# Kernel optimization log

Hardware: AMD Instinct MI355X
Metric: run time of the kernel (lower is better)

Reference implementation:

```python
import jax, jax.numpy as jnp
import numpy as np

D = 128           # volume / particle box size (pixels)
B = 8             # particles per batch
K = 125           # SO(3) grid poses (5x5x5 around each center Euler)
TOPK = 2          # keep_top_k_values
MAX_SHIFT_FRAC = 0.25  # main_config.projmatching.max_shift_fraction


def setup_inputs() -> dict:
    key = jax.random.key(0)
    k1, k2, k3, k4 = jax.random.split(key, 4)
    vol = jax.random.normal(k1, (D, D, D), dtype=jnp.float32)
    parts = jax.random.normal(k2, (B, D, D), dtype=jnp.float32)
    ctf = jax.random.uniform(k3, (B, D, D // 2 + 1), dtype=jnp.float32)
    euler_degs = jax.random.normal(k4, (K, 3), dtype=jnp.float32) * 8.0
    return {"vol": vol, "parts": parts, "ctf": ctf, "euler_degs": euler_degs}


def _rot_z(t):
    c, s = jnp.cos(t), jnp.sin(t)
    z, o = jnp.zeros_like(t), jnp.ones_like(t)
    return jnp.stack([jnp.stack([c, -s, z], -1),
                      jnp.stack([s, c, z], -1),
                      jnp.stack([z, z, o], -1)], -2)


def _rot_y(t):
    c, s = jnp.cos(t), jnp.sin(t)
    z, o = jnp.zeros_like(t), jnp.ones_like(t)
    return jnp.stack([jnp.stack([c, z, s], -1),
                      jnp.stack([z, o, z], -1),
                      jnp.stack([-s, z, c], -1)], -2)


def euler_zyz_to_matrix(degs):
    # RELION Euler convention ZYZ: R = Rz(a) @ Ry(b) @ Rz(c)
    rad = jnp.deg2rad(degs)
    return _rot_z(rad[..., 0]) @ _rot_y(rad[..., 1]) @ _rot_z(rad[..., 2])


def trilinear_sample(vol, zi, yi, xi):
    # vol: (Dz, Dy, W) complex64; coords: (K, h, w) float32 array indices
    Dz, Dy, W = vol.shape
    z0, y0, x0 = jnp.floor(zi), jnp.floor(yi), jnp.floor(xi)
    tz, ty, tx = zi - z0, yi - y0, xi - x0
    out = jnp.zeros(zi.shape, dtype=vol.dtype)
    for dz in (0, 1):
        wz = tz if dz else 1.0 - tz
        zc = z0 + dz
        vz = (zc >= 0) & (zc < Dz)
        zdx = jnp.clip(zc, 0, Dz - 1).astype(jnp.int32)
        for dy in (0, 1):
            wy = ty if dy else 1.0 - ty
            yc = y0 + dy
            vy = (yc >= 0) & (yc < Dy)
            ydx = jnp.clip(yc, 0, Dy - 1).astype(jnp.int32)
            for dx in (0, 1):
                wx = tx if dx else 1.0 - tx
                xc = x0 + dx
                vx = (xc >= 0) & (xc < W)
                xdx = jnp.clip(xc, 0, W - 1).astype(jnp.int32)
                w = jnp.where(vz & vy & vx, wz * wy * wx, 0.0)
                out = out + w * vol[zdx, ydx, xdx]
    return out


def project_fourier(vol_rfft, rotmats):
    # extract_central_slices_rfft: pose-dependent gather+trilinear interp of a
    # central slice from the fftshifted 3D rfft volume. Output: (K, D, D//2+1).
    d = D
    w = d // 2 + 1
    y = jnp.arange(d, dtype=jnp.float32) - d // 2   # fftshifted full-dim freqs (pixel units)
    x = jnp.arange(w, dtype=jnp.float32)            # rfft (non-negative) freqs
    yy, xx = jnp.meshgrid(y, x, indexing='ij')      # (d, w)
    coords = jnp.stack([xx, yy, jnp.zeros_like(yy)], -1)       # xyz, (d, w, 3), z = 0 plane
    rot = jnp.einsum('kij,hwj->khwi', rotmats, coords)          # (K, d, w, 3) rotated xyz
    conj_mask = rot[..., 0] < 0                                  # Hermitian symmetry: flip to x>=0 half
    rot = jnp.where(conj_mask[..., None], -rot, rot)
    xi = rot[..., 0]
    yi = rot[..., 1] + d // 2
    zi = rot[..., 2] + d // 2
    samples = trilinear_sample(vol_rfft, zi, yi, xi)
    samples = jnp.where(conj_mask, jnp.conj(samples), samples)
    r2 = xx ** 2 + yy ** 2                                       # zero beyond Nyquist radius
    samples = jnp.where(r2[None] > (d // 2) ** 2, 0.0, samples)
    return samples


def reference(vol, parts, ctf, euler_degs):
    # compute_dft: rfft volume, fftshift non-rfft dims
    vol_rfft = jnp.fft.fftshift(jnp.fft.rfftn(vol), axes=(0, 1))
    parts_rfft = jnp.fft.fftshift(jnp.fft.rfft2(parts), axes=(-2,))  # (B, D, W)
    rotmats = euler_zyz_to_matrix(euler_degs)                        # (K, 3, 3)
    projs = project_fourier(vol_rfft, rotmats)                       # (K, D, W)
    projs = ctf[:, None] * projs[None]                               # _apply_ctfF: (B, K, D, W)
    # correlate_dft_2d: cross-correlation via iFFT of parts * conj(projs)
    prod = parts_rfft[:, None] * jnp.conj(projs)
    prod = jnp.fft.ifftshift(prod, axes=(-2,))
    corr = jnp.fft.irfft2(prod, s=(D, D))                            # (B, K, D, D)
    corr = jnp.fft.fftshift(corr, axes=(-2, -1))                     # zero shift at center
    # _extract_ccor_max: restrict to |shift| <= max_shift_fraction*D, take top-k peaks
    center = D // 2
    max_shift = int(MAX_SHIFT_FRAC * D)
    idx = jnp.arange(D) - center
    win = (jnp.abs(idx)[:, None] <= max_shift) & (jnp.abs(idx)[None, :] <= max_shift)
    masked = jnp.where(win, corr, -jnp.inf)
    flat = masked.reshape(B, K, D * D)
    vals, top_idx = jax.lax.top_k(flat, TOPK)                        # (B, K, TOPK)
    shifts = jnp.stack([top_idx // D - center, top_idx % D - center], -1)  # (B, K, TOPK, 2) yx
    return vals, shifts
```

## Files before the change

### kernel.cpp

```cpp
#include <hip/hip_runtime.h>
#include <math.h>

#define D 128
#define W 65
#define NK 125
#define NB 8
#define SLAB (D*W)
#define TWO_PI 6.28318530717958647692f
#define R2C 0.70710678118654752440f
#define C8C 0.92387953251128675613f
#define S8C 0.38268343236508977173f


__device__ __forceinline__ bool better(float va, int ia, float vb, int ib) {
    return (va > vb) || (va == vb && ia < ib);
}
__device__ __forceinline__ float2 cmul(float2 a, float2 b) {
    return make_float2(a.x*b.x - a.y*b.y, a.x*b.y + a.y*b.x);
}
__device__ __forceinline__ void cmac(float2& acc, float2 a, float2 b) {
    acc.x = fmaf(a.x, b.x, fmaf(-a.y, b.y, acc.x));
    acc.y = fmaf(a.x, b.y, fmaf( a.y, b.x, acc.y));
}
__device__ __forceinline__ float2 cadd(float2 a, float2 b){ return make_float2(a.x+b.x, a.y+b.y); }
__device__ __forceinline__ float2 csub(float2 a, float2 b){ return make_float2(a.x-b.x, a.y-b.y); }

__device__ __forceinline__ void fft8_fwd(const float2* x, float2* a) {
    float2 e0 = x[0], o0 = x[1], e1 = x[2], o1 = x[3];
    float2 e2 = x[4], o2 = x[5], e3 = x[6], o3 = x[7];
    float2 t0 = cadd(e0, e2), t1 = csub(e0, e2);
    float2 t2 = cadd(e1, e3), t3 = csub(e1, e3);
    float2 E0 = cadd(t0, t2), E2 = csub(t0, t2);
    float2 E1 = make_float2(t1.x + t3.y, t1.y - t3.x);
    float2 E3 = make_float2(t1.x - t3.y, t1.y + t3.x);
    float2 u0 = cadd(o0, o2), u1 = csub(o0, o2);
    float2 u2 = cadd(o1, o3), u3 = csub(o1, o3);
    float2 O0 = cadd(u0, u2), O2 = csub(u0, u2);
    float2 O1 = make_float2(u1.x + u3.y, u1.y - u3.x);
    float2 O3 = make_float2(u1.x - u3.y, u1.y + u3.x);
    float2 w1 = make_float2(R2C*(O1.x + O1.y), R2C*(O1.y - O1.x));
    float2 w2 = make_float2(O2.y, -O2.x);
    float2 w3 = make_float2(R2C*(O3.y - O3.x), -R2C*(O3.x + O3.y));
    a[0] = cadd(E0, O0); a[4] = csub(E0, O0);
    a[1] = cadd(E1, w1); a[5] = csub(E1, w1);
    a[2] = cadd(E2, w2); a[6] = csub(E2, w2);
    a[3] = cadd(E3, w3); a[7] = csub(E3, w3);
}


template<int MODE>
__device__ __forceinline__ void fft128v2(const float* __restrict__ inf,
                                         const float2* __restrict__ inc,
                                         float2* __restrict__ out,
                                         int l0, int nlines,
                                         float2* __restrict__ Fl,
                                         float2* __restrict__ twf) {
    int tid = threadIdx.x;
    int line, t;
    if (MODE == 0) { t = tid & 7; line = tid >> 3; }
    else           { line = tid & 31; t = tid >> 5; }
    int l = l0 + line;
    bool live = (l < nlines);

    if (tid < 128) {
        float s, c;
        sincosf(-TWO_PI * (float)tid / 128.0f, &s, &c);
        twf[tid] = make_float2(c, s);
    }

    int base = 0, stride = 1;
    if (MODE == 1 || MODE == 3) { base = (l / W) * SLAB + (l % W); stride = W; }
    else if (MODE == 2) { base = l; stride = SLAB; }

    float2 xe[8], xo[8];
    if (live) {
        if (MODE == 0) {
            const float* r = inf + (size_t)l * D;
            #pragma unroll
            for (int j = 0; j < 8; ++j) {
                xe[j] = make_float2(r[t + 16*j], 0.f);
                xo[j] = make_float2(r[t + 8 + 16*j], 0.f);
            }
        } else {
            #pragma unroll
            for (int j = 0; j < 8; ++j) {
                xe[j] = inc[base + (t + 16*j) * stride];
                xo[j] = inc[base + (t + 8 + 16*j) * stride];
            }
        }
    } else {
        #pragma unroll
        for (int j = 0; j < 8; ++j) { xe[j] = make_float2(0,0); xo[j] = make_float2(0,0); }
    }
    float2 E[8], O[8];
    fft8_fwd(xe, E);
    fft8_fwd(xo, O);
    {
        const float2 w16[8] = {
            { 1.f, 0.f }, { C8C, -S8C }, { R2C, -R2C }, { S8C, -C8C },
            { 0.f, -1.f }, { -S8C, -C8C }, { -R2C, -R2C }, { -C8C, -S8C }
        };
        float2* Fp = Fl + line * 137 + t * 17;
        #pragma unroll
        for (int kk = 0; kk < 8; ++kk) {
            float2 wo = cmul(w16[kk], O[kk]);
            Fp[kk]     = cadd(E[kk], wo);
            Fp[kk + 8] = csub(E[kk], wo);
        }
    }
    __syncthreads();
    if (live) {
        const float2* Fr = Fl + line * 137;
        #pragma unroll
        for (int s = 0; s < 16; ++s) {
            int slot = t + 8 * s;
            if (MODE == 0 && slot > 64) break;
            int k = (MODE == 0) ? slot : (slot ^ 64);
            int kk = k & 15;
            float2 acc = make_float2(0.f, 0.f);
            #pragma unroll
            for (int tt = 0; tt < 8; ++tt) {
                cmac(acc, Fr[tt * 17 + kk], twf[(tt * k) & 127]);
            }
            if (MODE == 0)      out[(size_t)l * W + slot] = acc;
            else if (MODE == 3) out[(size_t)l * D + slot] = acc;
            else                out[base + slot * stride] = acc;
        }
    }
}


__global__ __launch_bounds__(256) void k1_kernel(const float* __restrict__ vol,
                                                 const float* __restrict__ parts,
                                                 const float* __restrict__ ctf,
                                                 const float* __restrict__ euler,
                                                 float2* __restrict__ bufA,
                                                 float2* __restrict__ pT1,
                                                 float* __restrict__ CT,
                                                 float* __restrict__ rot) {
    __shared__ float2 Fl[32 * 137];
    __shared__ float2 twf[128];
    int bid = blockIdx.x;
    int tid = threadIdx.x;
    if (bid < 512) {
        fft128v2<0>(vol, nullptr, bufA, bid * 32, D*D, Fl, twf);
    } else if (bid < 544) {
        fft128v2<0>(parts, nullptr, pT1, (bid - 512) * 32, NB*D, Fl, twf);
    } else if (bid == 544) {
        int k = tid;
        if (k < NK) {
            const float d2r = 0.017453292519943295f;
            float a = euler[k*3+0]*d2r, b = euler[k*3+1]*d2r, c = euler[k*3+2]*d2r;
            float sa, ca, sb, cb, sc, cc;
            sincosf(a, &sa, &ca); sincosf(b, &sb, &cb); sincosf(c, &sc, &cc);
            rot[k*9+0] =  ca*cb*cc - sa*sc;
            rot[k*9+1] = -ca*cb*sc - sa*cc;
            rot[k*9+2] =  ca*sb;
            rot[k*9+3] =  sa*cb*cc + ca*sc;
            rot[k*9+4] = -sa*cb*sc + ca*cc;
            rot[k*9+5] =  sa*sb;
            rot[k*9+6] = -sb*cc;
            rot[k*9+7] =  sb*sc;
            rot[k*9+8] =  cb;
        }
    } else {
        int i = (bid - 545) * 256 + tid;
        if (i < NB * W * D) {
            int m = i & (D-1);
            int t2 = i >> 7;
            int x = t2 % W;
            int b = t2 / W;
            CT[i] = ctf[b * SLAB + m * W + x];
        }
    }
}

__global__ __launch_bounds__(256) void k2_kernel(const float2* __restrict__ bufA,
                                                 float2* __restrict__ bufB,
                                                 const float2* __restrict__ pT1,
                                                 float2* __restrict__ QT) {
    __shared__ float2 Fl[32 * 137];
    __shared__ float2 twf[128];
    int bid = blockIdx.x;
    if (bid < 260) fft128v2<1>(nullptr, bufA, bufB, bid * 32, D*W, Fl, twf);
    else           fft128v2<3>(nullptr, pT1, QT, (bid - 260) * 32, NB*W, Fl, twf);
}

__global__ __launch_bounds__(256) void k3_kernel(const float2* __restrict__ bufB,
                                                 float2* __restrict__ bufA) {
    __shared__ float2 Fl[32 * 137];
    __shared__ float2 twf[128];
    fft128v2<2>(nullptr, bufB, bufA, blockIdx.x * 32, SLAB, Fl, twf);
}


__global__ void proj_kernel(const float2* __restrict__ vol, const float* __restrict__ rot,
                            float2* __restrict__ projT) {
    int idx = blockIdx.x * blockDim.x + threadIdx.x;
    if (idx >= NK * D * W) return;
    int h = idx & (D-1);
    int t2 = idx >> 7;
    int w = t2 % W;
    int k = t2 / W;
    float x = (float)w;
    float y = (float)(h - 64);
    const float* R = rot + k*9;
    float rx = R[0]*x + R[1]*y;
    float ry = R[3]*x + R[4]*y;
    float rz = R[6]*x + R[7]*y;
    bool neg = rx < 0.0f;
    if (neg) { rx = -rx; ry = -ry; rz = -rz; }
    float xi = rx;
    float yi = ry + 64.0f;
    float zi = rz + 64.0f;
    float z0 = floorf(zi), y0 = floorf(yi), x0 = floorf(xi);
    float tz = zi - z0, ty = yi - y0, tx = xi - x0;
    int z0i = (int)z0, y0i = (int)y0, x0i = (int)x0;
    float ar = 0.f, ai = 0.f;
    for (int dz = 0; dz < 2; ++dz) {
        float wz = dz ? tz : 1.0f - tz;
        int zc = z0i + dz;
        bool vz = (zc >= 0) && (zc < D);
        int zx = min(max(zc, 0), D-1);
        for (int dy = 0; dy < 2; ++dy) {
            float wy = dy ? ty : 1.0f - ty;
            int yc = y0i + dy;
            bool vy = (yc >= 0) && (yc < D);
            int yx = min(max(yc, 0), D-1);
            for (int dx = 0; dx < 2; ++dx) {
                float wx = dx ? tx : 1.0f - tx;
                int xc = x0i + dx;
                bool vx = (xc >= 0) && (xc < W);
                int xx = min(max(xc, 0), W-1);
                float wt = (vz && vy && vx) ? wz*wy*wx : 0.0f;
                float2 v = vol[zx * SLAB + yx * W + xx];
                ar = fmaf(wt, v.x, ar);
                ai = fmaf(wt, v.y, ai);
            }
        }
    }
    if (neg) ai = -ai;
    int yy = h - 64;
    if (w*w + yy*yy > 4096) { ar = 0.f; ai = 0.f; }
    projT[idx] = make_float2(ar, ai);
}


__global__ __launch_bounds__(256, 2) void corr_kernel(const float2* __restrict__ QT,
                                                      const float*  __restrict__ CT,
                                                      const float2* __restrict__ PJT,
                                                      float* __restrict__ outv) {
    __shared__ float2 tw[128];
    __shared__ float2 Ab[17*144];
    __shared__ float2 BC[32*67];
    __shared__ float  Ny[65];
    __shared__ float  redv[8];
    __shared__ int    redi[8];

    int bk = blockIdx.x;
    int b = bk / NK;
    int k = bk - b * NK;
    int tid = threadIdx.x;
    const float inv_d = 1.0f / 128.0f;

    if (tid < 128) {
        float s, c;
        sincosf(TWO_PI * (float)tid / 128.0f, &s, &c);
        tw[tid] = make_float2(c, s);
    }

    const float2* Qb = QT + b * (W * D);
    const float*  Cb = CT + b * (W * D);
    const float2* Jk = PJT + k * (W * D);

    int lane = tid & 63;
    int wv = tid >> 6;
    int sv = lane & 7;
    int vp = (96 + lane) & 127;
    float acc[16];
    #pragma unroll
    for (int j = 0; j < 16; ++j) acc[j] = 0.0f;
    float accR = 0.0f;
    int ur = 0, vr = 0;
    if (tid < 129) { if (tid < 65) { ur = 64; vr = tid; } else { ur = tid - 65; vr = 64; } }

    __syncthreads();

    float2 wvp = tw[vp];
    float2 tq = make_float2(1.0f, 0.0f);

    for (int cg = 0; cg < 4; ++cg) {
        int ncol = (cg == 0) ? 17 : 16;
        for (int i = tid; i < ncol * 16; i += 256) {
            int l = i >> 4, m0 = i & 15;
            int x = (l < 16) ? (4*cg + (l >> 2) + 16 * (l & 3)) : 64;
            const float2* Qx = Qb + x * 128 + m0;
            const float*  Cx = Cb + x * 128 + m0;
            const float2* Jx = Jk + x * 128 + m0;
            float2 p[8];
            #pragma unroll
            for (int j = 0; j < 8; ++j) {
                float2 qv = Qx[16*j];
                float  cf = Cx[16*j];
                float2 pj = Jx[16*j];
                float sx = qv.x * cf, sy = qv.y * cf;
                p[j] = make_float2(sx*pj.x + sy*pj.y, sy*pj.x - sx*pj.y);
            }
            float2 e0 = p[0], o0 = p[1], e1 = p[2], o1 = p[3];
            float2 e2 = p[4], o2 = p[5], e3 = p[6], o3 = p[7];
            float2 t0 = cadd(e0, e2), t1 = csub(e0, e2);
            float2 t2 = cadd(e1, e3), t3 = csub(e1, e3);
            float2 E0 = cadd(t0, t2), E2 = csub(t0, t2);
            float2 E1 = make_float2(t1.x - t3.y, t1.y + t3.x);
            float2 E3 = make_float2(t1.x + t3.y, t1.y - t3.x);
            float2 u0 = cadd(o0, o2), u1 = csub(o0, o2);
            float2 u2 = cadd(o1, o3), u3 = csub(o1, o3);
            float2 O0 = cadd(u0, u2), O2 = csub(u0, u2);
            float2 O1 = make_float2(u1.x - u3.y, u1.y + u3.x);
            float2 O3 = make_float2(u1.x + u3.y, u1.y - u3.x);
            float2 w1o = make_float2(R2C*(O1.x - O1.y), R2C*(O1.x + O1.y));
            float2 w2o = make_float2(-O2.y, O2.x);
            float2 w3o = make_float2(R2C*(-O3.x - O3.y), R2C*(O3.x - O3.y));
            float2* A = Ab + l * 144 + m0;
            A[0*18] = cadd(E0, O0);
            A[4*18] = csub(E0, O0);
            A[1*18] = cadd(E1, w1o);
            A[5*18] = csub(E1, w1o);
            A[2*18] = cadd(E2, w2o);
            A[6*18] = csub(E2, w2o);
            A[3*18] = cadd(E3, w3o);
            A[7*18] = csub(E3, w3o);
        }
        __syncthreads();
        {
            int lim = (cg == 0) ? 325 : 260;
            for (int i = tid; i < lim; i += 256) {
                if (i < 260) {
                    int q = i / 65;
                    int u2 = i - q * 65;
                    int r = u2 & 7, up = (96 + u2) & 127;
                    float2 wup = tw[up];
                    const float4* A0 = (const float4*)(Ab + (4*q+0)*144 + r*18);
                    const float4* A1 = (const float4*)(Ab + (4*q+1)*144 + r*18);
                    const float4* A2 = (const float4*)(Ab + (4*q+2)*144 + r*18);
                    const float4* A3 = (const float4*)(Ab + (4*q+3)*144 + r*18);
                    float2 g0{0,0}, g1{0,0}, g2{0,0}, g3{0,0};
                    float2 tc = make_float2(1.0f, 0.0f);
                    #pragma unroll
                    for (int h = 0; h < 8; ++h) {
                        float2 tA = tc;
                        float2 tB = cmul(tA, wup);
                        tc = cmul(tB, wup);
                        float4 a;
                        a = A0[h]; cmac(g0, make_float2(a.x,a.y), tA); cmac(g0, make_float2(a.z,a.w), tB);
                        a = A1[h]; cmac(g1, make_float2(a.x,a.y), tA); cmac(g1, make_float2(a.z,a.w), tB);
                        a = A2[h]; cmac(g2, make_float2(a.x,a.y), tA); cmac(g2, make_float2(a.z,a.w), tB);
                        a = A3[h]; cmac(g3, make_float2(a.x,a.y), tA); cmac(g3, make_float2(a.z,a.w), tB);
                    }
                    float sg = (u2 & 1) ? -inv_d : inv_d;
                    g0.x *= sg; g0.y *= sg; g1.x *= sg; g1.y *= sg;
                    g2.x *= sg; g2.y *= sg; g3.x *= sg; g3.y *= sg;
                    if (cg == 0 && q == 0) { g0.x *= 0.5f; g0.y *= 0.5f; }
                    float2 h0 = g0, h1 = g1, h2 = g2, h3 = g3;
                    const float sc = 2.0f * inv_d;
                    float2 p1 = make_float2(R2C*(h1.x - h1.y), R2C*(h1.x + h1.y));
                    float2 q1 = make_float2(R2C*(-h1.x - h1.y), R2C*(h1.x - h1.y));
                    float2 i1 = make_float2(-h1.y, h1.x);
                    float2 i2 = make_float2(-h2.y, h2.x);
                    float2 n2 = make_float2( h2.y, -h2.x);
                    float2 p3 = make_float2(R2C*(h3.x - h3.y), R2C*(h3.x + h3.y));
                    float2 q3 = make_float2(R2C*(-h3.x - h3.y), R2C*(h3.x - h3.y));
                    float2 i3 = make_float2(-h3.y, h3.x);
                    float2 a02 = cadd(h0, h2), s02 = csub(h0, h2);
                    float2 s0 = cadd(a02, cadd(h1, h3));
                    float2 s4 = csub(a02, cadd(h1, h3));
                    float2 s2 = cadd(s02, csub(i1, i3));
                    float2 s6 = csub(s02, csub(i1, i3));
                    float2 b0i = cadd(h0, i2);
                    float2 b0n = cadd(h0, n2);
                    float2 s1 = cadd(b0i, cadd(p1, q3));
                    float2 s5 = csub(b0i, cadd(p1, q3));
                    float2 s3 = cadd(b0n, cadd(q1, p3));
                    float2 s7 = csub(b0n, cadd(q1, p3));
                    float2* Bp = BC + q * (8*67) + u2;
                    Bp[0*67] = make_float2(s0.x*sc, s0.y*sc);
                    Bp[1*67] = make_float2(s1.x*sc, s1.y*sc);
                    Bp[2*67] = make_float2(s2.x*sc, s2.y*sc);
                    Bp[3*67] = make_float2(s3.x*sc, s3.y*sc);
                    Bp[4*67] = make_float2(s4.x*sc, s4.y*sc);
                    Bp[5*67] = make_float2(s5.x*sc, s5.y*sc);
                    Bp[6*67] = make_float2(s6.x*sc, s6.y*sc);
                    Bp[7*67] = make_float2(s7.x*sc, s7.y*sc);
                } else {
                    int u2 = i - 260;
                    int r = u2 & 7, up = (96 + u2) & 127;
                    float2 wup = tw[up];
                    const float4* A = (const float4*)(Ab + 16*144 + r*18);
                    float re = 0.0f;
                    float2 tc = make_float2(1.0f, 0.0f);
                    #pragma unroll
                    for (int h = 0; h < 8; ++h) {
                        float2 tA = tc;
                        float2 tB = cmul(tA, wup);
                        tc = cmul(tB, wup);
                        float4 a = A[h];
                        re = fmaf(a.x, tA.x, fmaf(-a.y, tA.y, re));
                        re = fmaf(a.z, tB.x, fmaf(-a.w, tB.y, re));
                    }
                    Ny[u2] = ((u2 & 1) ? -inv_d : inv_d) * re;
                }
            }
        }
        __syncthreads();
        {
            #pragma unroll
            for (int q = 0; q < 4; ++q) {
                const float2* Bq = BC + (q * 8 + sv) * 67 + wv * 16;
                float tx = tq.x, ty = tq.y;
                #pragma unroll
                for (int j = 0; j < 16; ++j) {
                    float2 bv = Bq[j];
                    acc[j] = fmaf(bv.x, tx, fmaf(-bv.y, ty, acc[j]));
                }
                tq = cmul(tq, wvp);
            }
            if (cg == 0) {
                float sgn = (lane & 1) ? -inv_d : inv_d;
                #pragma unroll
                for (int j = 0; j < 16; ++j) acc[j] = fmaf(sgn, Ny[wv * 16 + j], acc[j]);
            }
            if (tid < 129) {
                int sr = vr & 7, vpr = (96 + vr) & 127;
                float a = accR;
                #pragma unroll
                for (int q = 0; q < 4; ++q) {
                    float2 t = tw[((4*cg + q) * vpr) & 127];
                    float2 bv = BC[(q * 8 + sr) * 67 + ur];
                    a = fmaf(bv.x, t.x, fmaf(-bv.y, t.y, a));
                }
                if (cg == 0) a += (vr & 1) ? -inv_d * Ny[ur] : inv_d * Ny[ur];
                accR = a;
            }
        }
        __syncthreads();
    }

    float v1 = -INFINITY, v2 = -INFINITY;
    int i1 = 0x7fffffff, i2 = 0x7fffffff;
    #pragma unroll
    for (int j = 0; j < 16; ++j) {
        float val = acc[j];
        int uu = wv * 16 + j;
        int fl = (32 + uu) * D + (32 + lane);
        if (better(val, fl, v1, i1)) { v2 = v1; i2 = i1; v1 = val; i1 = fl; }
        else if (better(val, fl, v2, i2)) { v2 = val; i2 = fl; }
    }
    if (tid < 129) {
        int fl = (32 + ur) * D + (32 + vr);
        if (better(accR, fl, v1, i1)) { v2 = v1; i2 = i1; v1 = accR; i1 = fl; }
        else if (better(accR, fl, v2, i2)) { v2 = accR; i2 = fl; }
    }
    for (int off = 32; off > 0; off >>= 1) {
        float b1 = __shfl_down(v1, off); int j1 = __shfl_down(i1, off);
        float b2 = __shfl_down(v2, off); int j2 = __shfl_down(i2, off);
        if (better(b1, j1, v1, i1)) {
            float nv2; int ni2;
            if (better(v1, i1, b2, j2)) { nv2 = v1; ni2 = i1; } else { nv2 = b2; ni2 = j2; }
            v1 = b1; i1 = j1; v2 = nv2; i2 = ni2;
        } else {
            if (better(b1, j1, v2, i2)) { v2 = b1; i2 = j1; }
        }
    }
    int wave = tid >> 6;
    if ((tid & 63) == 0) {
        redv[wave*2]   = v1; redi[wave*2]   = i1;
        redv[wave*2+1] = v2; redi[wave*2+1] = i2;
    }
    __syncthreads();
    if (tid == 0) {
        float r1 = -INFINITY, r2 = -INFINITY;
        int q1 = 0x7fffffff, q2 = 0x7fffffff;
        for (int i = 0; i < 8; ++i) {
            float val = redv[i]; int fl = redi[i];
            if (better(val, fl, r1, q1)) { r2 = r1; q2 = q1; r1 = val; q1 = fl; }
            else if (better(val, fl, r2, q2)) { r2 = val; q2 = fl; }
        }
        int base = bk * 2;
        outv[base]     = r1;
        outv[base + 1] = r2;
        float* os = outv + NB*NK*2;
        os[(base    )*2 + 0] = (float)(q1 / D - 64);
        os[(base    )*2 + 1] = (float)(q1 % D - 64);
        os[(base + 1)*2 + 0] = (float)(q2 / D - 64);
        os[(base + 1)*2 + 1] = (float)(q2 % D - 64);
    }
}


extern "C" void kernel_launch(void* const* d_in, const int* in_sizes, int n_in,
                              void* d_out, int out_size, void* d_ws, size_t ws_size,
                              hipStream_t stream) {
    const float* vol   = (const float*)d_in[0];
    const float* parts = (const float*)d_in[1];
    const float* ctf   = (const float*)d_in[2];
    const float* euler = (const float*)d_in[3];
    float* out = (float*)d_out;

    const int VOLC = D * SLAB;
    float2* bufA   = (float2*)d_ws;
    float2* bufB   = bufA + VOLC;
    float2* pT1    = bufB + VOLC;
    float2* QT     = pT1 + NB * SLAB;
    float2* PJT    = QT + NB * W * D;
    float*  CT     = (float*)(PJT + NK * W * D);
    float*  rot    = CT + NB * W * D;

    k1_kernel<<<805, 256, 0, stream>>>(vol, parts, ctf, euler, bufA, pT1, CT, rot);
    k2_kernel<<<277, 256, 0, stream>>>(bufA, bufB, pT1, QT);
    k3_kernel<<<260, 256, 0, stream>>>(bufB, bufA);
    proj_kernel<<<(NK*D*W + 255) / 256, 256, 0, stream>>>(bufA, rot, PJT);
    corr_kernel<<<NB * NK, 256, 0, stream>>>(QT, CT, PJT, out);
}
```

Measured before the change: 92.95 us.

## Prefetch next column group into registers and remap blocks for L2 reuse

The corr kernel now loads the Q, CTF and projection values for the next column group into registers right after the barrier, so the global loads overlap the DFT stage that works from shared memory. Block indices are remapped so that consecutive blocks share the same projection k across the batch index, which is meant to improve L2 reuse of the projection data. The twiddle recurrence now steps by the squared twiddle, which shortens the dependency chain. The register prefetch raises register pressure under launch_bounds(256,2) and could cause spills.

```diff
diff --git a/kernel.cpp b/kernel.cpp
--- a/kernel.cpp
+++ b/kernel.cpp
@@ -45,6 +45,34 @@
     a[1] = cadd(E1, w1); a[5] = csub(E1, w1);
     a[2] = cadd(E2, w2); a[6] = csub(E2, w2);
     a[3] = cadd(E3, w3); a[7] = csub(E3, w3);
+}
+
+__device__ __forceinline__ void ifft8_store(float2* __restrict__ Ab, const float2* p,
+                                            int l, int m0) {
+    float2 e0 = p[0], o0 = p[1], e1 = p[2], o1 = p[3];
+    float2 e2 = p[4], o2 = p[5], e3 = p[6], o3 = p[7];
+    float2 t0 = cadd(e0, e2), t1 = csub(e0, e2);
+    float2 t2 = cadd(e1, e3), t3 = csub(e1, e3);
+    float2 E0 = cadd(t0, t2), E2 = csub(t0, t2);
+    float2 E1 = make_float2(t1.x - t3.y, t1.y + t3.x);
+    float2 E3 = make_float2(t1.x + t3.y, t1.y - t3.x);
+    float2 u0 = cadd(o0, o2), u1 = csub(o0, o2);
+    float2 u2 = cadd(o1, o3), u3 = csub(o1, o3);
+    float2 O0 = cadd(u0, u2), O2 = csub(u0, u2);
+    float2 O1 = make_float2(u1.x - u3.y, u1.y + u3.x);
+    float2 O3 = make_float2(u1.x + u3.y, u1.y - u3.x);
+    float2 w1o = make_float2(R2C*(O1.x - O1.y), R2C*(O1.x + O1.y));
+    float2 w2o = make_float2(-O2.y, O2.x);
+    float2 w3o = make_float2(R2C*(-O3.x - O3.y), R2C*(O3.x - O3.y));
+    float2* A = Ab + l * 144 + m0;
+    A[0*18] = cadd(E0, O0);
+    A[4*18] = csub(E0, O0);
+    A[1*18] = cadd(E1, w1o);
+    A[5*18] = csub(E1, w1o);
+    A[2*18] = cadd(E2, w2o);
+    A[6*18] = csub(E2, w2o);
+    A[3*18] = cadd(E3, w3o);
+    A[7*18] = csub(E3, w3o);
 }
 
 
@@ -257,9 +285,10 @@
     __shared__ float  redv[8];
     __shared__ int    redi[8];
 
-    int bk = blockIdx.x;
-    int b = bk / NK;
-    int k = bk - b * NK;
+    int g = blockIdx.x;
+    int logical = (g & 7) * 125 + (g >> 3);
+    int k = logical >> 3;
+    int b = logical & 7;
     int tid = threadIdx.x;
     const float inv_d = 1.0f / 128.0f;
 
@@ -289,49 +318,50 @@
     float2 wvp = tw[vp];
     float2 tq = make_float2(1.0f, 0.0f);
 
+    int l1 = tid >> 4, m01 = tid & 15;
+    float2 Qv[8]; float Cv[8]; float2 Jv[8];
+
     for (int cg = 0; cg < 4; ++cg) {
-        int ncol = (cg == 0) ? 17 : 16;
-        for (int i = tid; i < ncol * 16; i += 256) {
-            int l = i >> 4, m0 = i & 15;
-            int x = (l < 16) ? (4*cg + (l >> 2) + 16 * (l & 3)) : 64;
-            const float2* Qx = Qb + x * 128 + m0;
-            const float*  Cx = Cb + x * 128 + m0;
-            const float2* Jx = Jk + x * 128 + m0;
+        if (cg == 0) {
+            for (int i = tid; i < 17 * 16; i += 256) {
+                int l = i >> 4, m0 = i & 15;
+                int x = (l < 16) ? ((l >> 2) + 16 * (l & 3)) : 64;
+                const float2* Qx = Qb + x * 128 + m0;
+                const float*  Cx = Cb + x * 128 + m0;
+                const float2* Jx = Jk + x * 128 + m0;
+                float2 p[8];
+                #pragma unroll
+                for (int j = 0; j < 8; ++j) {
+                    float2 qv = Qx[16*j];
+                    float  cf = Cx[16*j];
+                    float2 pj = Jx[16*j];
+                    float sx = qv.x * cf, sy = qv.y * cf;
+                    p[j] = make_float2(sx*pj.x + sy*pj.y, sy*pj.x - sx*pj.y);
+                }
+                ifft8_store(Ab, p, l, m0);
+            }
+        } else {
             float2 p[8];
             #pragma unroll
             for (int j = 0; j < 8; ++j) {
-                float2 qv = Qx[16*j];
-                float  cf = Cx[16*j];
-                float2 pj = Jx[16*j];
-                float sx = qv.x * cf, sy = qv.y * cf;
-                p[j] = make_float2(sx*pj.x + sy*pj.y, sy*pj.x - sx*pj.y);
-            }
-            float2 e0 = p[0], o0 = p[1], e1 = p[2], o1 = p[3];
-            float2 e2 = p[4], o2 = p[5], e3 = p[6], o3 = p[7];
-            float2 t0 = cadd(e0, e2), t1 = csub(e0, e2);
-            float2 t2 = cadd(e1, e3), t3 = csub(e1, e3);
-            float2 E0 = cadd(t0, t2), E2 = csub(t0, t2);
-            float2 E1 = make_float2(t1.x - t3.y, t1.y + t3.x);
-            float2 E3 = make_float2(t1.x + t3.y, t1.y - t3.x);
-            float2 u0 = cadd(o0, o2), u1 = csub(o0, o2);
-            float2 u2 = cadd(o1, o3), u3 = csub(o1, o3);
-            float2 O0 = cadd(u0, u2), O2 = csub(u0, u2);
-            float2 O1 = make_float2(u1.x - u3.y, u1.y + u3.x);
-            float2 O3 = make_float2(u1.x + u3.y, u1.y - u3.x);
-            float2 w1o = make_float2(R2C*(O1.x - O1.y), R2C*(O1.x + O1.y));
-            float2 w2o = make_float2(-O2.y, O2.x);
-            float2 w3o = make_float2(R2C*(-O3.x - O3.y), R2C*(O3.x - O3.y));
-            float2* A = Ab + l * 144 + m0;
-            A[0*18] = cadd(E0, O0);
-            A[4*18] = csub(E0, O0);
-            A[1*18] = cadd(E1, w1o);
-            A[5*18] = csub(E1, w1o);
-            A[2*18] = cadd(E2, w2o);
-            A[6*18] = csub(E2, w2o);
-            A[3*18] = cadd(E3, w3o);
-            A[7*18] = csub(E3, w3o);
+                float sx = Qv[j].x * Cv[j], sy = Qv[j].y * Cv[j];
+                p[j] = make_float2(sx*Jv[j].x + sy*Jv[j].y, sy*Jv[j].x - sx*Jv[j].y);
+            }
+            ifft8_store(Ab, p, l1, m01);
         }
         __syncthreads();
+        if (cg < 3) {
+            int xn = 4*(cg+1) + (l1 >> 2) + 16 * (l1 & 3);
+            const float2* Qx = Qb + xn * 128 + m01;
+            const float*  Cx = Cb + xn * 128 + m01;
+            const float2* Jx = Jk + xn * 128 + m01;
+            #pragma unroll
+            for (int j = 0; j < 8; ++j) {
+                Qv[j] = Qx[16*j];
+                Cv[j] = Cx[16*j];
+                Jv[j] = Jx[16*j];
+            }
+        }
         {
             int lim = (cg == 0) ? 325 : 260;
             for (int i = tid; i < lim; i += 256) {
@@ -340,22 +370,22 @@
                     int u2 = i - q * 65;
                     int r = u2 & 7, up = (96 + u2) & 127;
                     float2 wup = tw[up];
+                    float2 wup2 = cmul(wup, wup);
                     const float4* A0 = (const float4*)(Ab + (4*q+0)*144 + r*18);
                     const float4* A1 = (const float4*)(Ab + (4*q+1)*144 + r*18);
                     const float4* A2 = (const float4*)(Ab + (4*q+2)*144 + r*18);
                     const float4* A3 = (const float4*)(Ab + (4*q+3)*144 + r*18);
                     float2 g0{0,0}, g1{0,0}, g2{0,0}, g3{0,0};
-                    float2 tc = make_float2(1.0f, 0.0f);
+                    float2 tA = make_float2(1.0f, 0.0f);
                     #pragma unroll
                     for (int h = 0; h < 8; ++h) {
-                        float2 tA = tc;
                         float2 tB = cmul(tA, wup);
-                        tc = cmul(tB, wup);
                         float4 a;
                         a = A0[h]; cmac(g0, make_float2(a.x,a.y), tA); cmac(g0, make_float2(a.z,a.w), tB);
                         a = A1[h]; cmac(g1, make_float2(a.x,a.y), tA); cmac(g1, make_float2(a.z,a.w), tB);
                         a = A2[h]; cmac(g2, make_float2(a.x,a.y), tA); cmac(g2, make_float2(a.z,a.w), tB);
                         a = A3[h]; cmac(g3, make_float2(a.x,a.y), tA); cmac(g3, make_float2(a.z,a.w), tB);
+                        tA = cmul(tA, wup2);
                     }
                     float sg = (u2 & 1) ? -inv_d : inv_d;
                     g0.x *= sg; g0.y *= sg; g1.x *= sg; g1.y *= sg;
@@ -395,17 +425,17 @@
                     int u2 = i - 260;
                     int r = u2 & 7, up = (96 + u2) & 127;
                     float2 wup = tw[up];
+                    float2 wup2 = cmul(wup, wup);
                     const float4* A = (const float4*)(Ab + 16*144 + r*18);
                     float re = 0.0f;
-                    float2 tc = make_float2(1.0f, 0.0f);
+                    float2 tA = make_float2(1.0f, 0.0f);
                     #pragma unroll
                     for (int h = 0; h < 8; ++h) {
-                        float2 tA = tc;
                         float2 tB = cmul(tA, wup);
-                        tc = cmul(tB, wup);
                         float4 a = A[h];
                         re = fmaf(a.x, tA.x, fmaf(-a.y, tA.y, re));
                         re = fmaf(a.z, tB.x, fmaf(-a.w, tB.y, re));
+                        tA = cmul(tA, wup2);
                     }
                     Ny[u2] = ((u2 & 1) ? -inv_d : inv_d) * re;
                 }
@@ -485,7 +515,7 @@
             if (better(val, fl, r1, q1)) { r2 = r1; q2 = q1; r1 = val; q1 = fl; }
             else if (better(val, fl, r2, q2)) { r2 = val; q2 = fl; }
         }
-        int base = bk * 2;
+        int base = (b * NK + k) * 2;
         outv[base]     = r1;
         outv[base + 1] = r2;
         float* os = outv + NB*NK*2;
```

New measurement: 91.95 us. Within noise of the previous version (-1.1%).
